# Optimization experiments

Hardware: AMD Instinct MI355X
Metric: run time of the kernel (lower is better)

The kernel has to match this reference:

```python
import jax, jax.numpy as jnp
import numpy as np

B, TQ, TK = 2, 2048, 2048
H, E, D = 16, 256, 4096       # num_heads, embed_dim, d_model
DH = D // H                   # head_dim == embed_dim (required by per-head RMSNorm(embed_dim))
LAMBDA_INIT = 0.8
LAYER_INDEX = 0
EPS = 1.1920929e-07           # torch RMSNorm default eps = finfo(float32).eps


def setup_inputs() -> dict:
    key = jax.random.key(0)
    ks = jax.random.split(key, 14)
    s = 0.02
    lam_init_val = LAMBDA_INIT - 0.6 * float(np.exp(-0.3 * LAYER_INDEX))
    return {
        "x": jax.random.normal(ks[0], (B, TQ, E), jnp.float32),
        "encoder_out": jax.random.normal(ks[1], (B, TK, E), jnp.float32),
        "Wq": jax.random.normal(ks[2], (H, E, DH), jnp.float32) * s,
        "bq": jnp.zeros((H, DH), jnp.float32),
        "Wk": jax.random.normal(ks[3], (H, E, DH), jnp.float32) * s,
        "bk": jnp.zeros((H, DH), jnp.float32),
        "Wv": jax.random.normal(ks[4], (H, E, DH), jnp.float32) * s,
        "bv": jnp.zeros((H, DH), jnp.float32),
        "lq1": jax.random.normal(ks[5], (H, DH), jnp.float32) * 0.1,
        "lk1": jax.random.normal(ks[6], (H, DH), jnp.float32) * 0.1,
        "lq2": jax.random.normal(ks[7], (H, DH), jnp.float32) * 0.1,
        "lk2": jax.random.normal(ks[8], (H, DH), jnp.float32) * 0.1,
        "lam_init": jnp.full((H,), lam_init_val, jnp.float32),
        "g": jnp.ones((H, DH), jnp.float32),     # per-head RMSNorm weight
        "Wo": jax.random.normal(ks[9], (D, E), jnp.float32) * s,
        "bo": jnp.zeros((E,), jnp.float32),
    }


def reference(x, encoder_out, Wq, bq, Wk, bk, Wv, bv,
              lq1, lk1, lq2, lk2, lam_init, g, Wo, bo):
    # per-head projections, vectorized over heads: [B,H,T,DH]
    q = jnp.einsum('bte,hed->bhtd', x, Wq) + bq[:, None, :]
    k = jnp.einsum('bse,hed->bhsd', encoder_out, Wk) + bk[:, None, :]
    v = jnp.einsum('bse,hed->bhsd', encoder_out, Wv) + bv[:, None, :]
    dh2 = DH // 2
    q1, q2 = q[..., :dh2], q[..., dh2:]
    k1, k2 = k[..., :dh2], k[..., dh2:]
    scale = 1.0 / jnp.sqrt(jnp.float32(dh2))
    s1 = jax.nn.softmax(jnp.einsum('bhtd,bhsd->bhts', q1, k1) * scale, axis=-1)
    s2 = jax.nn.softmax(jnp.einsum('bhtd,bhsd->bhts', q2, k2) * scale, axis=-1)
    # learned per-head lambda scalar
    lam = jnp.exp(jnp.sum(lq1 * lk1, axis=-1)) - jnp.exp(jnp.sum(lq2 * lk2, axis=-1)) + lam_init  # [H]
    w = s1 - lam[None, :, None, None] * s2
    o = jnp.einsum('bhts,bhsd->bhtd', w, v)
    # per-head RMSNorm + (1 - lambda_init) scaling
    rms = jnp.sqrt(jnp.mean(o * o, axis=-1, keepdims=True) + EPS)
    o = (1.0 - LAMBDA_INIT) * (o / rms) * g[None, :, None, :]
    # concat heads -> output projection
    o = o.transpose(0, 2, 1, 3).reshape(B, TQ, D)
    return o @ Wo + bo
```

## Files before the change

### kernel.cpp

```cpp
#include <hip/hip_runtime.h>
#include <hip/hip_bf16.h>
#include <stdint.h>
#include <math.h>

typedef __bf16 bf16;
typedef __bf16 bf16x8 __attribute__((ext_vector_type(8)));
typedef float f32x4 __attribute__((ext_vector_type(4)));
typedef float f32x16 __attribute__((ext_vector_type(16)));
typedef unsigned int u32;

#define MFMA16(a, b, c) __builtin_amdgcn_mfma_f32_16x16x32_bf16(a, b, c, 0, 0, 0)
#define MFMA32(a, b, c) __builtin_amdgcn_mfma_f32_32x32x16_bf16(a, b, c, 0, 0, 0)

typedef const u32 __attribute__((address_space(1)))* gptr1;
typedef u32 __attribute__((address_space(3)))* lptr3;

__device__ __forceinline__ void load_lds16(const void* g, void* l) {
    __builtin_amdgcn_global_load_lds((gptr1)g, (lptr3)l, 16, 0, 0);
}

__device__ __forceinline__ u32 pk2(float lo, float hi_) {
    union { bf16 h[2]; u32 u; } t;
    t.h[0] = (bf16)lo; t.h[1] = (bf16)hi_;
    return t.u;
}

#define SCALE_QK 0.08838834764831845f
#define LOG2E 1.4426950408889634f
#define QK_PRESCALE (SCALE_QK * LOG2E)
#define RMS_EPS 1.1920929e-07f
#define OUT_SCALE 0.2f
#define M0_BIAS (-16.0f)

__global__ void cvt_act(const float* __restrict__ x, const float* __restrict__ enc,
                        bf16* __restrict__ xb, bf16* __restrict__ eb) {
    int gid = blockIdx.x * 256 + threadIdx.x;
    const float* src = (gid < 131072) ? x : enc;
    bf16* dst = (gid < 131072) ? xb : eb;
    int i = (gid & 131071) * 8;
    float4 v0 = *(const float4*)(src + i);
    float4 v1 = *(const float4*)(src + i + 4);
    union { bf16 h[8]; uint4 u; } p;
    p.h[0] = (bf16)v0.x; p.h[1] = (bf16)v0.y; p.h[2] = (bf16)v0.z; p.h[3] = (bf16)v0.w;
    p.h[4] = (bf16)v1.x; p.h[5] = (bf16)v1.y; p.h[6] = (bf16)v1.z; p.h[7] = (bf16)v1.w;
    *(uint4*)(dst + i) = p.u;
}

__global__ void txp_w(const float* __restrict__ Wq, const float* __restrict__ Wk,
                      const float* __restrict__ Wv,
                      bf16* __restrict__ WTq, bf16* __restrict__ WTk, bf16* __restrict__ WTv) {
    int z = blockIdx.z; int iw = z >> 4, hh = z & 15;
    const float* src = (iw == 0 ? Wq : iw == 1 ? Wk : Wv) + hh * 65536;
    bf16* dst = (iw == 0 ? WTq : iw == 1 ? WTk : WTv) + hh * 65536;
    __shared__ bf16 T[64][68];
    int r0 = blockIdx.y * 64, c0 = blockIdx.x * 64;
    int tid = threadIdx.x;
#pragma unroll
    for (int t = 0; t < 4; ++t) {
        int idx = tid + t * 256;
        int row = idx >> 4, c4 = (idx & 15) * 4;
        float4 v = *(const float4*)(src + (r0 + row) * 256 + c0 + c4);
        T[row][c4] = (bf16)v.x; T[row][c4 + 1] = (bf16)v.y;
        T[row][c4 + 2] = (bf16)v.z; T[row][c4 + 3] = (bf16)v.w;
    }
    __syncthreads();
#pragma unroll
    for (int t = 0; t < 2; ++t) {
        int idx = tid + t * 256;
        int crow = idx >> 3, r8 = (idx & 7) * 8;
        union { bf16 h[8]; uint4 u; } p;
#pragma unroll
        for (int j = 0; j < 8; ++j) p.h[j] = T[r8 + j][crow];
        *(uint4*)(dst + (c0 + crow) * 256 + r0 + r8) = p.u;
    }
}

__global__ void txp_wo(const float* __restrict__ Wo, bf16* __restrict__ WoT) {
    __shared__ bf16 T[64][68];
    int r0 = blockIdx.y * 64, c0 = blockIdx.x * 64;
    int tid = threadIdx.x;
#pragma unroll
    for (int t = 0; t < 4; ++t) {
        int idx = tid + t * 256;
        int row = idx >> 4, c4 = (idx & 15) * 4;
        float4 v = *(const float4*)(Wo + (size_t)(r0 + row) * 256 + c0 + c4);
        T[row][c4] = (bf16)v.x; T[row][c4 + 1] = (bf16)v.y;
        T[row][c4 + 2] = (bf16)v.z; T[row][c4 + 3] = (bf16)v.w;
    }
    __syncthreads();
#pragma unroll
    for (int t = 0; t < 2; ++t) {
        int idx = tid + t * 256;
        int crow = idx >> 3, r8 = (idx & 7) * 8;
        union { bf16 h[8]; uint4 u; } p;
#pragma unroll
        for (int j = 0; j < 8; ++j) p.h[j] = T[r8 + j][crow];
        *(uint4*)(WoT + (size_t)(c0 + crow) * 4096 + r0 + r8) = p.u;
    }
}

__global__ void lam_kernel(const float* __restrict__ lq1, const float* __restrict__ lk1,
                           const float* __restrict__ lq2, const float* __restrict__ lk2,
                           const float* __restrict__ lam_init, float* __restrict__ lam_out) {
    int tid = threadIdx.x; int hh = tid >> 4, i = tid & 15;
    float s1 = 0.f, s2 = 0.f;
#pragma unroll
    for (int j = 0; j < 16; ++j) {
        int d = i + j * 16;
        s1 += lq1[hh * 256 + d] * lk1[hh * 256 + d];
        s2 += lq2[hh * 256 + d] * lk2[hh * 256 + d];
    }
#pragma unroll
    for (int msk = 1; msk < 16; msk <<= 1) { s1 += __shfl_xor(s1, msk); s2 += __shfl_xor(s2, msk); }
    if (i == 0) lam_out[hh] = __expf(s1) - __expf(s2) + lam_init[hh];
}

__global__ __launch_bounds__(256) void proj_gemm(
    const bf16* __restrict__ xb, const bf16* __restrict__ eb,
    const bf16* __restrict__ WTq, const bf16* __restrict__ WTk, const bf16* __restrict__ WTv,
    const float* __restrict__ bq, const float* __restrict__ bk, const float* __restrict__ bv,
    bf16* __restrict__ Qb, bf16* __restrict__ Kb, bf16* __restrict__ VTb) {
    int z = blockIdx.z;
    const bf16* A = (z == 0) ? xb : eb;
    const bf16* BT = (z == 0) ? WTq : (z == 1) ? WTk : WTv;
    const float* bias = (z == 0) ? bq : (z == 1) ? bk : bv;
    bf16* out = (z == 0) ? Qb : Kb;
    float qs = (z == 0) ? QK_PRESCALE : 1.0f;

    __shared__ alignas(16) bf16 As[128 * 32];
    __shared__ alignas(16) bf16 Bs[128 * 32];
    int m0 = blockIdx.x * 128, n0 = blockIdx.y * 128;
    int tid = threadIdx.x, w = tid >> 6, lane = tid & 63;
    int lrow = lane & 15, lgrp = lane >> 4, lk8 = lgrp * 8;
    int wr = (w >> 1) * 64, wc = (w & 1) * 64;

    f32x4 acc[4][4];
#pragma unroll
    for (int i = 0; i < 4; ++i)
#pragma unroll
        for (int j = 0; j < 4; ++j) acc[i][j] = (f32x4){0.f, 0.f, 0.f, 0.f};

    for (int k0 = 0; k0 < 256; k0 += 32) {
        __syncthreads();
#pragma unroll
        for (int t = 0; t < 2; ++t) {
            int c = tid + t * 256;
            int row = c >> 2, k8 = (c & 3) * 8;
            load_lds16(A + (m0 + row) * 256 + k0 + k8, &As[c * 8]);
            load_lds16(BT + (n0 + row) * 256 + k0 + k8, &Bs[c * 8]);
        }
        __syncthreads();
        bf16x8 af[4], bfr[4];
#pragma unroll
        for (int f = 0; f < 4; ++f) af[f] = *(const bf16x8*)&As[(wr + f * 16 + lrow) * 32 + lk8];
#pragma unroll
        for (int f = 0; f < 4; ++f) bfr[f] = *(const bf16x8*)&Bs[(wc + f * 16 + lrow) * 32 + lk8];
#pragma unroll
        for (int i = 0; i < 4; ++i)
#pragma unroll
            for (int j = 0; j < 4; ++j) acc[i][j] = MFMA16(af[i], bfr[j], acc[i][j]);
    }

    if (z == 2) {
        int lg2 = ((lgrp & 1) << 1) | (lgrp >> 1);
#pragma unroll
        for (int i = 0; i < 4; ++i) {
            int m_ = m0 + wr + i * 16;
            int bb = m_ >> 11, tb = m_ & 2047;
#pragma unroll
            for (int j = 0; j < 4; ++j) {
                int n = n0 + wc + j * 16 + lrow;
                float bvv = bias[n];
                int hh = n >> 8, d = n & 255;
                union { bf16 h[4]; uint2 u2; } pk;
#pragma unroll
                for (int r = 0; r < 4; ++r) pk.h[r] = (bf16)(acc[i][j][r] + bvv);
                *(uint2*)(VTb + (((size_t)bb * 16 + hh) * 256 + d) * 2048 + tb + lg2 * 4) = pk.u2;
            }
        }
    } else {
#pragma unroll
        for (int i = 0; i < 4; ++i) {
#pragma unroll
            for (int j = 0; j < 4; ++j) {
                int n = n0 + wc + j * 16 + lrow;
                float bvv = bias[n];
                int hh = n >> 8, d = n & 255;
#pragma unroll
                for (int r = 0; r < 4; ++r) {
                    int m = m0 + wr + i * 16 + lgrp * 4 + r;
                    int bb = m >> 11, tt = m & 2047;
                    out[(((size_t)bb * 16 + hh) * 2048 + tt) * 256 + d] = (bf16)((acc[i][j][r] + bvv) * qs);
                }
            }
        }
    }
}

__global__ __launch_bounds__(256, 2) void attn_kernel(
    const bf16* __restrict__ Qb, const bf16* __restrict__ Kb, const bf16* __restrict__ VTb,
    const float* __restrict__ lam_ws, const float* __restrict__ g, bf16* __restrict__ On) {
    __shared__ alignas(16) char SMEM[75264];
    bf16* KsB = (bf16*)SMEM;
    bf16* VsB = (bf16*)(SMEM + 32768);
    float* o2buf  = (float*)SMEM;
    float* smem_i = (float*)(SMEM + 65536);
    float* smem_r = (float*)(SMEM + 66048);
    float* psum   = (float*)(SMEM + 66560);

    int orig = blockIdx.x;
    int xcd = orig & 7, idx = orig >> 3;
    int bh = xcd * 4 + (idx >> 5);
    int qb = idx & 31;
    int b = bh >> 4, h = bh & 15;
    int q0 = qb * 64;

    int tid = threadIdx.x, w = tid >> 6, lane = tid & 63;
    int lq = lane & 31, hi = lane >> 5;
    int br = w >> 1, qw = (w & 1) * 32;
    int ksw = lq & 7;
    int vsw = (lq >> 1) & 3;

    const bf16* Qg = Qb + ((size_t)bh * 2048 + q0 + qw + lq) * 256 + br * 128;
    bf16x8 qf[8];
#pragma unroll
    for (int dk = 0; dk < 8; ++dk)
        qf[dk] = *(const bf16x8*)(Qg + dk * 16 + hi * 8);

    f32x16 o[8];
#pragma unroll
    for (int dt = 0; dt < 8; ++dt)
#pragma unroll
        for (int i = 0; i < 16; ++i) o[dt][i] = 0.f;
    float lsum = 0.f;

    const bf16* Kg = Kb + (size_t)bh * 2048 * 256;
    const bf16* VTg = VTb + (size_t)bh * 256 * 2048;

    auto STAGE = [&](int buf, int kt) {
        int s0 = kt * 32;
#pragma unroll
        for (int i = 0; i < 4; ++i) {
            int s = i * 256 + tid;
            int row = s >> 5;
            int cg = (s & 31) ^ (row & 7);
            load_lds16(Kg + (size_t)(s0 + row) * 256 + cg * 8, KsB + buf * 8192 + s * 8);
        }
#pragma unroll
        for (int i = 0; i < 4; ++i) {
            int s = i * 256 + tid;
            int row = s >> 2;
            int cg = (s & 3) ^ ((row >> 1) & 3);
            load_lds16(VTg + (size_t)row * 2048 + s0 + cg * 8, VsB + buf * 8192 + s * 8);
        }
    };

    STAGE(0, 0);
    __syncthreads();

    int cur = 0;
    for (int kt = 0; kt < 64; ++kt) {
        if (kt + 1 < 64) STAGE(cur ^ 1, kt + 1);
        const bf16* Kbuf = KsB + cur * 8192;
        const bf16* Vbuf = VsB + cur * 8192;

        f32x16 sa, sb;
#pragma unroll
        for (int i = 0; i < 16; ++i) { sa[i] = M0_BIAS; sb[i] = 0.f; }
        __builtin_amdgcn_s_setprio(1);
#pragma unroll
        for (int dk = 0; dk < 4; ++dk) {
            bf16x8 k0 = *(const bf16x8*)&Kbuf[lq * 256 + (((br * 16 + 4 * dk + hi) ^ ksw) << 3)];
            bf16x8 k1 = *(const bf16x8*)&Kbuf[lq * 256 + (((br * 16 + 4 * dk + 2 + hi) ^ ksw) << 3)];
            sa = MFMA32(k0, qf[2 * dk], sa);
            sb = MFMA32(k1, qf[2 * dk + 1], sb);
        }
        __builtin_amdgcn_s_setprio(0);

        float p[16];
        float ls0 = 0.f, ls1 = 0.f;
#pragma unroll
        for (int i = 0; i < 8; ++i) { p[i] = exp2f(sa[i] + sb[i]); ls0 += p[i]; }
#pragma unroll
        for (int i = 8; i < 16; ++i) { p[i] = exp2f(sa[i] + sb[i]); ls1 += p[i]; }
        lsum += ls0 + ls1;

        union { u32 u[4]; bf16x8 v; } PA0, PA1;
        PA0.u[0] = pk2(p[0], p[1]);   PA0.u[1] = pk2(p[2], p[3]);
        PA0.u[2] = pk2(p[4], p[5]);   PA0.u[3] = pk2(p[6], p[7]);
        PA1.u[0] = pk2(p[8], p[9]);   PA1.u[1] = pk2(p[10], p[11]);
        PA1.u[2] = pk2(p[12], p[13]); PA1.u[3] = pk2(p[14], p[15]);

        __builtin_amdgcn_s_setprio(1);
#pragma unroll
        for (int dt = 0; dt < 8; ++dt) {
            const bf16* vrow = &Vbuf[(dt * 32 + lq) * 32];
            bf16x8 v0 = *(const bf16x8*)&vrow[(hi ^ vsw) << 3];
            o[dt] = MFMA32(PA0.v, v0, o[dt]);
            bf16x8 v1 = *(const bf16x8*)&vrow[((2 + hi) ^ vsw) << 3];
            o[dt] = MFMA32(PA1.v, v1, o[dt]);
        }
        __builtin_amdgcn_s_setprio(0);

        __syncthreads();
        cur ^= 1;
    }

    lsum += __shfl_xor(lsum, 32);
    float lam = lam_ws[h];
    float inv = (br == 0) ? 1.f / lsum : lam / lsum;
    smem_i[br * 64 + qw + lq] = inv;
    __syncthreads();

    if (br == 1) {
#pragma unroll
        for (int r = 0; r < 16; ++r) {
            int qp = (r & 3) + 8 * (r >> 2) + 4 * hi + qw;
            float i2 = smem_i[64 + qp];
#pragma unroll
            for (int dt = 0; dt < 8; ++dt)
                o2buf[qp * 256 + dt * 32 + lq] = o[dt][r] * i2;
        }
    }
    __syncthreads();

    if (br == 0) {
#pragma unroll
        for (int r = 0; r < 16; ++r) {
            int qp = (r & 3) + 8 * (r >> 2) + 4 * hi + qw;
            float i1 = smem_i[qp];
            float ss = 0.f;
#pragma unroll
            for (int dt = 0; dt < 8; ++dt) {
                float v = o[dt][r] * i1 - o2buf[qp * 256 + dt * 32 + lq];
                o[dt][r] = v;
                ss += v * v;
            }
            psum[qp * 33 + lq] = ss;
        }
    }
    __syncthreads();

    if (tid < 64) {
        float s = 0.f;
#pragma unroll
        for (int i = 0; i < 32; ++i) s += psum[tid * 33 + i];
        smem_r[tid] = 1.f / sqrtf(s * (1.f / 256.f) + RMS_EPS);
    }
    __syncthreads();

    if (br == 0) {
        float gv[8];
#pragma unroll
        for (int dt = 0; dt < 8; ++dt) gv[dt] = g[h * 256 + dt * 32 + lq] * OUT_SCALE;
#pragma unroll
        for (int r = 0; r < 16; ++r) {
            int qp = (r & 3) + 8 * (r >> 2) + 4 * hi + qw;
            float rv = smem_r[qp];
            size_t base = ((size_t)b * 2048 + q0 + qp) * 4096 + h * 256;
#pragma unroll
            for (int dt = 0; dt < 8; ++dt)
                On[base + dt * 32 + lq] = (bf16)(o[dt][r] * rv * gv[dt]);
        }
    }
}

__global__ __launch_bounds__(256) void out_gemm(const bf16* __restrict__ A, const bf16* __restrict__ BT,
                                                const float* __restrict__ bo, float* __restrict__ out) {
    __shared__ alignas(16) bf16 As[64 * 32];
    __shared__ alignas(16) bf16 Bs[64 * 32];
    int m0 = blockIdx.x * 64, n0 = blockIdx.y * 64;
    int tid = threadIdx.x, w = tid >> 6, lane = tid & 63;
    int lrow = lane & 15, lgrp = lane >> 4, lk8 = lgrp * 8;
    int wr = (w >> 1) * 32, wc = (w & 1) * 32;
    f32x4 acc[2][2];
#pragma unroll
    for (int i = 0; i < 2; ++i)
#pragma unroll
        for (int j = 0; j < 2; ++j) acc[i][j] = (f32x4){0.f, 0.f, 0.f, 0.f};
    for (int k0 = 0; k0 < 4096; k0 += 32) {
        __syncthreads();
        int row = tid >> 2, k8 = (tid & 3) * 8;
        load_lds16(A + (size_t)(m0 + row) * 4096 + k0 + k8, &As[tid * 8]);
        load_lds16(BT + (size_t)(n0 + row) * 4096 + k0 + k8, &Bs[tid * 8]);
        __syncthreads();
        bf16x8 af[2], bfr[2];
#pragma unroll
        for (int f = 0; f < 2; ++f) {
            af[f] = *(const bf16x8*)&As[(wr + f * 16 + lrow) * 32 + lk8];
            bfr[f] = *(const bf16x8*)&Bs[(wc + f * 16 + lrow) * 32 + lk8];
        }
#pragma unroll
        for (int i = 0; i < 2; ++i)
#pragma unroll
            for (int j = 0; j < 2; ++j) acc[i][j] = MFMA16(af[i], bfr[j], acc[i][j]);
    }
#pragma unroll
    for (int i = 0; i < 2; ++i)
#pragma unroll
        for (int j = 0; j < 2; ++j) {
            int n = n0 + wc + j * 16 + lrow;
            float bv = bo[n];
#pragma unroll
            for (int r = 0; r < 4; ++r) {
                int m = m0 + wr + i * 16 + lgrp * 4 + r;
                out[(size_t)m * 256 + n] = acc[i][j][r] + bv;
            }
        }
}

extern "C" void kernel_launch(void* const* d_in, const int* in_sizes, int n_in,
                              void* d_out, int out_size, void* d_ws, size_t ws_size,
                              hipStream_t stream) {
    const float* x = (const float*)d_in[0];
    const float* enc = (const float*)d_in[1];
    const float* Wq = (const float*)d_in[2];
    const float* bq = (const float*)d_in[3];
    const float* Wk = (const float*)d_in[4];
    const float* bk = (const float*)d_in[5];
    const float* Wv = (const float*)d_in[6];
    const float* bv = (const float*)d_in[7];
    const float* lq1 = (const float*)d_in[8];
    const float* lk1 = (const float*)d_in[9];
    const float* lq2 = (const float*)d_in[10];
    const float* lk2 = (const float*)d_in[11];
    const float* lam_init = (const float*)d_in[12];
    const float* g = (const float*)d_in[13];
    const float* Wo = (const float*)d_in[14];
    const float* bo = (const float*)d_in[15];
    float* out = (float*)d_out;

    char* ws = (char*)d_ws;
    const size_t MB = 1024 * 1024;
    bf16* xb  = (bf16*)(ws + 0 * MB);
    bf16* eb  = (bf16*)(ws + 2 * MB);
    bf16* WTq = (bf16*)(ws + 4 * MB);
    bf16* WTk = (bf16*)(ws + 6 * MB);
    bf16* WTv = (bf16*)(ws + 8 * MB);
    bf16* WoT = (bf16*)(ws + 10 * MB);
    float* lam = (float*)(ws + 12 * MB);
    bf16* Qb  = (bf16*)(ws + 13 * MB);
    bf16* Kb  = (bf16*)(ws + 45 * MB);
    bf16* On  = (bf16*)(ws + 77 * MB);
    bf16* VTb = (bf16*)(ws + 109 * MB);

    hipLaunchKernelGGL(cvt_act, dim3(1024), dim3(256), 0, stream, x, enc, xb, eb);
    hipLaunchKernelGGL(txp_w, dim3(4, 4, 48), dim3(256), 0, stream, Wq, Wk, Wv, WTq, WTk, WTv);
    hipLaunchKernelGGL(txp_wo, dim3(4, 64, 1), dim3(256), 0, stream, Wo, WoT);
    hipLaunchKernelGGL(lam_kernel, dim3(1), dim3(256), 0, stream, lq1, lk1, lq2, lk2, lam_init, lam);
    hipLaunchKernelGGL(proj_gemm, dim3(32, 32, 3), dim3(256), 0, stream,
                       xb, eb, WTq, WTk, WTv, bq, bk, bv, Qb, Kb, VTb);
    hipLaunchKernelGGL(attn_kernel, dim3(1024), dim3(256), 0, stream, Qb, Kb, VTb, lam, g, On);
    hipLaunchKernelGGL(out_gemm, dim3(64, 4), dim3(256), 0, stream, On, WoT, bo, out);
}
```

Before: 349.2 us.

## Use 512-thread attention blocks sharing K/V tiles with four-stage async pipeline

The attention kernel now runs 512-thread blocks that cover 128 query rows, so two 64-row groups share each staged K/V tile. Staging moves from double buffering with a full barrier per step to a four-buffer ring that prefetches three tiles ahead, gated by explicit vmcnt waits plus s_barrier. The goal is to halve redundant K/V global loads per query and hide load latency. In exchange each block needs about 140KB of LDS and one block per CU, and the epilogue runs serially for the two halves with extra barriers.

```diff
diff --git a/kernel.cpp b/kernel.cpp
--- a/kernel.cpp
+++ b/kernel.cpp
@@ -197,27 +197,27 @@
     }
 }
 
-__global__ __launch_bounds__(256, 2) void attn_kernel(
+__global__ __launch_bounds__(512, 1) void attn_kernel(
     const bf16* __restrict__ Qb, const bf16* __restrict__ Kb, const bf16* __restrict__ VTb,
     const float* __restrict__ lam_ws, const float* __restrict__ g, bf16* __restrict__ On) {
-    __shared__ alignas(16) char SMEM[75264];
+    __shared__ alignas(16) char SMEM[140800];
     bf16* KsB = (bf16*)SMEM;
-    bf16* VsB = (bf16*)(SMEM + 32768);
+    bf16* VsB = (bf16*)(SMEM + 65536);
     float* o2buf  = (float*)SMEM;
-    float* smem_i = (float*)(SMEM + 65536);
-    float* smem_r = (float*)(SMEM + 66048);
-    float* psum   = (float*)(SMEM + 66560);
+    float* smem_i = (float*)(SMEM + 131072);
+    float* smem_r = (float*)(SMEM + 132096);
+    float* psum   = (float*)(SMEM + 132352);
 
     int orig = blockIdx.x;
     int xcd = orig & 7, idx = orig >> 3;
-    int bh = xcd * 4 + (idx >> 5);
-    int qb = idx & 31;
+    int bh = xcd * 4 + (idx >> 4);
+    int qb = idx & 15;
     int b = bh >> 4, h = bh & 15;
-    int q0 = qb * 64;
 
     int tid = threadIdx.x, w = tid >> 6, lane = tid & 63;
     int lq = lane & 31, hi = lane >> 5;
-    int br = w >> 1, qw = (w & 1) * 32;
+    int br = (w >> 1) & 1, qw = (w & 1) * 32, qh = w >> 2;
+    int q0 = qb * 128 + qh * 64;
     int ksw = lq & 7;
     int vsw = (lq >> 1) & 3;
 
@@ -240,15 +240,15 @@
     auto STAGE = [&](int buf, int kt) {
         int s0 = kt * 32;
 #pragma unroll
-        for (int i = 0; i < 4; ++i) {
-            int s = i * 256 + tid;
+        for (int i = 0; i < 2; ++i) {
+            int s = i * 512 + tid;
             int row = s >> 5;
             int cg = (s & 31) ^ (row & 7);
             load_lds16(Kg + (size_t)(s0 + row) * 256 + cg * 8, KsB + buf * 8192 + s * 8);
         }
 #pragma unroll
-        for (int i = 0; i < 4; ++i) {
-            int s = i * 256 + tid;
+        for (int i = 0; i < 2; ++i) {
+            int s = i * 512 + tid;
             int row = s >> 2;
             int cg = (s & 3) ^ ((row >> 1) & 3);
             load_lds16(VTg + (size_t)row * 2048 + s0 + cg * 8, VsB + buf * 8192 + s * 8);
@@ -256,13 +256,17 @@
     };
 
     STAGE(0, 0);
-    __syncthreads();
-
-    int cur = 0;
+    STAGE(1, 1);
+    STAGE(2, 2);
+
     for (int kt = 0; kt < 64; ++kt) {
-        if (kt + 1 < 64) STAGE(cur ^ 1, kt + 1);
-        const bf16* Kbuf = KsB + cur * 8192;
-        const bf16* Vbuf = VsB + cur * 8192;
+        if (kt < 62)       asm volatile("s_waitcnt vmcnt(8)\ns_barrier" ::: "memory");
+        else if (kt == 62) asm volatile("s_waitcnt vmcnt(4)\ns_barrier" ::: "memory");
+        else               asm volatile("s_waitcnt vmcnt(0)\ns_barrier" ::: "memory");
+        if (kt + 3 < 64) STAGE((kt + 3) & 3, kt + 3);
+
+        const bf16* Kbuf = KsB + (kt & 3) * 8192;
+        const bf16* Vbuf = VsB + (kt & 3) * 8192;
 
         f32x16 sa, sb;
 #pragma unroll
@@ -301,67 +305,66 @@
             o[dt] = MFMA32(PA1.v, v1, o[dt]);
         }
         __builtin_amdgcn_s_setprio(0);
-
-        __syncthreads();
-        cur ^= 1;
-    }
+    }
+    __syncthreads();
 
     lsum += __shfl_xor(lsum, 32);
     float lam = lam_ws[h];
     float inv = (br == 0) ? 1.f / lsum : lam / lsum;
-    smem_i[br * 64 + qw + lq] = inv;
+    smem_i[br * 128 + qh * 64 + qw + lq] = inv;
     __syncthreads();
 
-    if (br == 1) {
-#pragma unroll
-        for (int r = 0; r < 16; ++r) {
-            int qp = (r & 3) + 8 * (r >> 2) + 4 * hi + qw;
-            float i2 = smem_i[64 + qp];
-#pragma unroll
-            for (int dt = 0; dt < 8; ++dt)
-                o2buf[qp * 256 + dt * 32 + lq] = o[dt][r] * i2;
-        }
-    }
-    __syncthreads();
-
-    if (br == 0) {
-#pragma unroll
-        for (int r = 0; r < 16; ++r) {
-            int qp = (r & 3) + 8 * (r >> 2) + 4 * hi + qw;
-            float i1 = smem_i[qp];
-            float ss = 0.f;
-#pragma unroll
-            for (int dt = 0; dt < 8; ++dt) {
-                float v = o[dt][r] * i1 - o2buf[qp * 256 + dt * 32 + lq];
-                o[dt][r] = v;
-                ss += v * v;
-            }
-            psum[qp * 33 + lq] = ss;
-        }
-    }
-    __syncthreads();
-
-    if (tid < 64) {
-        float s = 0.f;
-#pragma unroll
-        for (int i = 0; i < 32; ++i) s += psum[tid * 33 + i];
-        smem_r[tid] = 1.f / sqrtf(s * (1.f / 256.f) + RMS_EPS);
-    }
-    __syncthreads();
-
-    if (br == 0) {
-        float gv[8];
-#pragma unroll
-        for (int dt = 0; dt < 8; ++dt) gv[dt] = g[h * 256 + dt * 32 + lq] * OUT_SCALE;
-#pragma unroll
-        for (int r = 0; r < 16; ++r) {
-            int qp = (r & 3) + 8 * (r >> 2) + 4 * hi + qw;
-            float rv = smem_r[qp];
-            size_t base = ((size_t)b * 2048 + q0 + qp) * 4096 + h * 256;
-#pragma unroll
-            for (int dt = 0; dt < 8; ++dt)
-                On[base + dt * 32 + lq] = (bf16)(o[dt][r] * rv * gv[dt]);
-        }
+    float gv[8];
+#pragma unroll
+    for (int dt = 0; dt < 8; ++dt) gv[dt] = g[h * 256 + dt * 32 + lq] * OUT_SCALE;
+
+    for (int hp = 0; hp < 2; ++hp) {
+        if (qh == hp && br == 1) {
+#pragma unroll
+            for (int r = 0; r < 16; ++r) {
+                int qp = (r & 3) + 8 * (r >> 2) + 4 * hi + qw;
+                float i2 = smem_i[128 + qh * 64 + qp];
+#pragma unroll
+                for (int dt = 0; dt < 8; ++dt)
+                    o2buf[qp * 256 + dt * 32 + lq] = o[dt][r] * i2;
+            }
+        }
+        __syncthreads();
+        if (qh == hp && br == 0) {
+#pragma unroll
+            for (int r = 0; r < 16; ++r) {
+                int qp = (r & 3) + 8 * (r >> 2) + 4 * hi + qw;
+                float i1 = smem_i[qh * 64 + qp];
+                float ss = 0.f;
+#pragma unroll
+                for (int dt = 0; dt < 8; ++dt) {
+                    float v = o[dt][r] * i1 - o2buf[qp * 256 + dt * 32 + lq];
+                    o[dt][r] = v;
+                    ss += v * v;
+                }
+                psum[qp * 33 + lq] = ss;
+            }
+        }
+        __syncthreads();
+        if (tid < 64) {
+            float s = 0.f;
+#pragma unroll
+            for (int i = 0; i < 32; ++i) s += psum[tid * 33 + i];
+            smem_r[tid] = 1.f / sqrtf(s * (1.f / 256.f) + RMS_EPS);
+        }
+        __syncthreads();
+        if (qh == hp && br == 0) {
+#pragma unroll
+            for (int r = 0; r < 16; ++r) {
+                int qp = (r & 3) + 8 * (r >> 2) + 4 * hi + qw;
+                float rv = smem_r[qp];
+                size_t base = ((size_t)b * 2048 + q0 + qp) * 4096 + h * 256;
+#pragma unroll
+                for (int dt = 0; dt < 8; ++dt)
+                    On[base + dt * 32 + lq] = (bf16)(o[dt][r] * rv * gv[dt]);
+            }
+        }
+        __syncthreads();
     }
 }
 
@@ -450,6 +453,6 @@
     hipLaunchKernelGGL(lam_kernel, dim3(1), dim3(256), 0, stream, lq1, lk1, lq2, lk2, lam_init, lam);
     hipLaunchKernelGGL(proj_gemm, dim3(32, 32, 3), dim3(256), 0, stream,
                        xb, eb, WTq, WTk, WTv, bq, bk, bv, Qb, Kb, VTb);
-    hipLaunchKernelGGL(attn_kernel, dim3(1024), dim3(256), 0, stream, Qb, Kb, VTb, lam, g, On);
+    hipLaunchKernelGGL(attn_kernel, dim3(512), dim3(512), 0, stream, Qb, Kb, VTb, lam, g, On);
     hipLaunchKernelGGL(out_gemm, dim3(64, 4), dim3(256), 0, stream, On, WoT, bo, out);
 }
```

Result: no change. 343.1 us (-1.7%).
